# Kernel optimization log

Hardware: AMD Instinct MI355X
Metric: run time of the kernel (lower is better)

The kernel has to match this reference:

```python
import jax, jax.numpy as jnp
import numpy as np

N, M, E = 100000, 500, 300000
XS, GS, OUT, HEADS = 100, 100, 100, 2
SLOPE = 0.2
EPS = 1e-12


def l2norm(x, axis):
    n = jnp.linalg.norm(x, axis=axis, keepdims=True)
    return x / jnp.maximum(n, EPS)


def gat_layer(h_ijk, ends, n, W, att):
    # W: [heads*out, in_dim] (no bias); att: [1, heads, out]
    heads, out = att.shape[1], att.shape[2]
    c = (h_ijk @ W.T).reshape(-1, heads, out)               # [E, H, D]
    a = jnp.sum(att * c, axis=2, keepdims=True)             # [E, H, 1]
    e = jnp.exp(-jax.nn.leaky_relu(a, SLOPE))
    denom = jax.ops.segment_sum(e, ends, num_segments=n)    # [n, H, 1]
    alpha = e / denom[ends]                                 # segment softmax (dropout=eval/identity)
    h = jax.ops.segment_sum(alpha * c, ends, num_segments=n)  # [n, H, D]
    h = jax.nn.elu(h)
    h = l2norm(h, axis=2)
    return h.reshape(n, heads * out)


def merge_layer(h_in, h_out, Wi, bi, Wo, bo, Wl, bl):
    hi = h_in @ Wi.T + bi
    ho = h_out @ Wo.T + bo
    lam = jax.nn.sigmoid(jnp.concatenate([hi, ho], axis=1) @ Wl.T + bl)
    h = lam * hi + (1.0 - lam) * ho
    return l2norm(jax.nn.elu(h), axis=1)


def setup_inputs() -> dict:
    key = jax.random.key(0)
    ks = jax.random.split(key, 24)
    D = HEADS * OUT  # 200
    in1 = 2 * XS + GS   # 300
    in2 = 3 * D         # 600
    s = 0.05
    return {
        'edge_idx': jax.random.randint(ks[0], (2, E), 0, N),
        'edge_type': jax.random.randint(ks[1], (E,), 0, M),
        'path_idx': jax.random.randint(ks[2], (2, 8), 0, N),
        'path_type': jax.random.randint(ks[3], (2, 8), 0, M),
        'use_path': 0,
        'x': jax.random.normal(ks[4], (N, XS), jnp.float32),
        'g': jax.random.normal(ks[5], (M, GS), jnp.float32),
        'W_in1': s * jax.random.normal(ks[6], (D, in1), jnp.float32),
        'att_in1': s * jax.random.normal(ks[7], (1, HEADS, OUT), jnp.float32),
        'W_out1': s * jax.random.normal(ks[8], (D, in1), jnp.float32),
        'att_out1': s * jax.random.normal(ks[9], (1, HEADS, OUT), jnp.float32),
        'Wi1': s * jax.random.normal(ks[10], (D, D), jnp.float32), 'bi1': jnp.zeros((D,), jnp.float32),
        'Wo1': s * jax.random.normal(ks[11], (D, D), jnp.float32), 'bo1': jnp.zeros((D,), jnp.float32),
        'Wl1': s * jax.random.normal(ks[12], (1, 2 * D), jnp.float32), 'bl1': jnp.zeros((1,), jnp.float32),
        'Wr': s * jax.random.normal(ks[13], (D, GS), jnp.float32), 'br': jnp.zeros((D,), jnp.float32),
        'Wf': s * jax.random.normal(ks[14], (D, in1), jnp.float32), 'bf': jnp.zeros((D,), jnp.float32),
        'W_in2': s * jax.random.normal(ks[15], (D, in2), jnp.float32),
        'att_in2': s * jax.random.normal(ks[16], (1, 1, D), jnp.float32),
        'W_out2': s * jax.random.normal(ks[17], (D, in2), jnp.float32),
        'att_out2': s * jax.random.normal(ks[18], (1, 1, D), jnp.float32),
        'Wi2': s * jax.random.normal(ks[19], (D, D), jnp.float32), 'bi2': jnp.zeros((D,), jnp.float32),
        'Wo2': s * jax.random.normal(ks[20], (D, D), jnp.float32), 'bo2': jnp.zeros((D,), jnp.float32),
        'Wl2': s * jax.random.normal(ks[21], (1, 2 * D), jnp.float32), 'bl2': jnp.zeros((1,), jnp.float32),
        'W_ent': s * jax.random.normal(ks[22], (D, XS), jnp.float32),
    }


def reference(edge_idx, edge_type, path_idx, path_type, use_path, x, g,
              W_in1, att_in1, W_out1, att_out1, Wi1, bi1, Wo1, bo1, Wl1, bl1,
              Wr, br, Wf, bf,
              W_in2, att_in2, W_out2, att_out2, Wi2, bi2, Wo2, bo2, Wl2, bl2,
              W_ent):
    n, m = x.shape[0], g.shape[0]
    x = l2norm(x, axis=1)  # x_initial is renormalized each forward
    row, col = edge_idx[0], edge_idx[1]
    # hop 1: gather-concat per-edge features [E, 2*XS+GS]
    h_ijk = jnp.concatenate([x[row], x[col], g[edge_type]], axis=1)
    h_in = gat_layer(h_ijk, col, n, W_in1, att_in1)
    h_out = gat_layer(h_ijk, row, n, W_out1, att_out1)
    h = merge_layer(h_in, h_out, Wi1, bi1, Wo1, bo1, Wl1, bl1)
    # relation layer
    g_edges = jax.ops.segment_sum(h_ijk, edge_type, num_segments=m)
    g_edges = jax.nn.elu(l2norm(g_edges, axis=1))
    g_prime = (g @ Wr.T + br) + (g_edges @ Wf.T + bf)
    # hop 2
    h_ijk2 = jnp.concatenate([h[row], h[col], g_prime[edge_type]], axis=1)
    h_in2 = gat_layer(h_ijk2, col, n, W_in2, att_in2)
    h_out2 = gat_layer(h_ijk2, row, n, W_out2, att_out2)
    h = merge_layer(h_in2, h_out2, Wi2, bi2, Wo2, bo2, Wl2, bl2)
    # entity residual layer
    h_prime = x @ W_ent.T + h
    return h_prime
```

## Files before the change

kernel.cpp:

```cpp
#include <hip/hip_runtime.h>
#include <cstddef>
#include <cstdint>

#define WSLOPE 0.2f
#define WEPS 1e-12f

typedef __attribute__((ext_vector_type(8))) short bf16x8;
typedef __attribute__((ext_vector_type(4))) float f32x4;
typedef __attribute__((ext_vector_type(2))) float f32x2;

__device__ __forceinline__ float waveSum(float v) {
#pragma unroll
    for (int off = 32; off > 0; off >>= 1) v += __shfl_xor(v, off, 64);
    return v;
}
__device__ __forceinline__ float rowSum16(float v) {
#pragma unroll
    for (int off = 8; off > 0; off >>= 1) v += __shfl_xor(v, off, 64);
    return v;
}
__device__ __forceinline__ float eluf(float v) { return v > 0.f ? v : expm1f(v); }
__device__ __forceinline__ short f2bf(float f) {
    union { float f; uint32_t u; } v; v.f = f;
    uint32_t r = v.u + 0x7FFF + ((v.u >> 16) & 1);
    return (short)(r >> 16);
}
__device__ __forceinline__ float bf2f(short s) {
    union { uint32_t u; float f; } v; v.u = ((uint32_t)(uint16_t)s) << 16;
    return v.f;
}

__global__ void k_nodeprep(const float* __restrict__ x, short* __restrict__ xnb,
                           const float* __restrict__ wai, const float* __restrict__ wao,
                           f32x4* __restrict__ ndi, f32x4* __restrict__ ndo, int N) {
    int wid = blockIdx.x * 4 + (threadIdx.x >> 6);
    int lane = threadIdx.x & 63;
    if (wid >= N) return;
    const float* p = x + (size_t)wid * 100;
    float a0 = p[lane];
    float a1 = (lane < 36) ? p[lane + 64] : 0.f;
    float ss = waveSum(a0 * a0 + a1 * a1);
    float inv = 1.f / fmaxf(sqrtf(ss), WEPS);
    float f0 = a0 * inv, f1 = a1 * inv;
    short* xb = xnb + (size_t)wid * 112;
    xb[lane] = f2bf(f0);
    if (lane < 36) xb[64 + lane] = f2bf(f1);
    else if (lane < 48) xb[64 + lane] = 0;
    float rI[2], cI[2], rO[2], cO[2];
#pragma unroll
    for (int h = 0; h < 2; ++h) {
        const float* wi = wai + h * 300;
        const float* wo = wao + h * 300;
        float ri = f0 * wi[lane] + f1 * wi[lane + 64];
        float ci = f0 * wi[100 + lane] + f1 * wi[100 + lane + 64];
        float ro = f0 * wo[lane] + f1 * wo[lane + 64];
        float co = f0 * wo[100 + lane] + f1 * wo[100 + lane + 64];
        rI[h] = waveSum(ri); cI[h] = waveSum(ci); rO[h] = waveSum(ro); cO[h] = waveSum(co);
    }
    if (lane == 0) {
        ndi[wid] = f32x4{rI[0], rI[1], cI[0], cI[1]};
        ndo[wid] = f32x4{rO[0], rO[1], cO[0], cO[1]};
    }
}

__global__ void k_gprep(const float* __restrict__ g, short* __restrict__ gbf,
                        short* __restrict__ gcomb,
                        const float* __restrict__ wai, const float* __restrict__ wao,
                        float* __restrict__ gdi, float* __restrict__ gdo, int M) {
    int m = blockIdx.x * 4 + (threadIdx.x >> 6);
    int lane = threadIdx.x & 63;
    if (m >= M) return;
    const float* gm = g + (size_t)m * 100;
    float v0 = gm[lane];
    float v1 = (lane < 36) ? gm[lane + 64] : 0.f;
    short b0 = f2bf(v0), b1 = (lane < 36) ? f2bf(v1) : (short)0;
    short* gb = gbf + (size_t)m * 112;
    gb[lane] = b0;
    if (lane < 48) gb[64 + lane] = (lane < 36) ? b1 : (short)0;
    short* gc = gcomb + (size_t)m * 416;
    gc[lane] = b0;
    if (lane < 48) gc[64 + lane] = (lane < 36) ? b1 : (short)0;
    float s0 = v0 * wai[200 + lane];
    float s1 = v0 * wai[500 + lane];
    float s2 = v0 * wao[200 + lane];
    float s3 = v0 * wao[500 + lane];
    if (lane < 36) {
        s0 += v1 * wai[264 + lane]; s1 += v1 * wai[564 + lane];
        s2 += v1 * wao[264 + lane]; s3 += v1 * wao[564 + lane];
    }
    s0 = waveSum(s0); s1 = waveSum(s1); s2 = waveSum(s2); s3 = waveSum(s3);
    if (lane == 0) { gdi[m * 2] = s0; gdi[m * 2 + 1] = s1; gdo[m * 2] = s2; gdo[m * 2 + 1] = s3; }
}

__global__ void k_count(const int* __restrict__ keys, int* __restrict__ cnt, int n) {
    int i = blockIdx.x * 256 + threadIdx.x;
    if (i < n) atomicAdd(&cnt[keys[i]], 1);
}

#define SCAN_CHUNK 2048
__global__ void k_blocksum(const int* __restrict__ cnt, int* __restrict__ bsum, int n) {
    __shared__ int sh[256];
    int b = blockIdx.x, t = threadIdx.x;
    int base = b * SCAN_CHUNK;
    int s = 0;
    for (int i = t; i < SCAN_CHUNK; i += 256) { int idx = base + i; if (idx < n) s += cnt[idx]; }
    sh[t] = s; __syncthreads();
    for (int off = 128; off > 0; off >>= 1) { if (t < off) sh[t] += sh[t + off]; __syncthreads(); }
    if (t == 0) bsum[b] = sh[0];
}

__global__ void k_scanwrite(const int* __restrict__ cnt, const int* __restrict__ bsum,
                            int* __restrict__ offs, int* __restrict__ cur, int n, int nb) {
    __shared__ int sh[256];
    __shared__ int sbase;
    int b = blockIdx.x, t = threadIdx.x;
    if (t == 0) { int s = 0; for (int i = 0; i < b; ++i) s += bsum[i]; sbase = s; }
    __syncthreads();
    int base = b * SCAN_CHUNK;
    int loc[8]; int ts = 0;
#pragma unroll
    for (int i = 0; i < 8; ++i) { int idx = base + t * 8 + i; int v = (idx < n) ? cnt[idx] : 0; loc[i] = ts; ts += v; }
    sh[t] = ts; __syncthreads();
    for (int off = 1; off < 256; off <<= 1) {
        int v = (t >= off) ? sh[t - off] : 0;
        __syncthreads();
        sh[t] += v;
        __syncthreads();
    }
    int excl = (t == 0) ? 0 : sh[t - 1];
    int gbase = sbase + excl;
#pragma unroll
    for (int i = 0; i < 8; ++i) {
        int idx = base + t * 8 + i;
        if (idx < n) { offs[idx] = gbase + loc[i]; cur[idx] = gbase + loc[i]; }
    }
    if (b == nb - 1 && t == 255) offs[n] = sbase + sh[255];
}

__global__ void k_scatter3(const int* __restrict__ keys, const int* __restrict__ other,
                           const int* __restrict__ et, int* __restrict__ cur,
                           int* __restrict__ nbrS, int* __restrict__ etS,
                           int* __restrict__ keyS, int n) {
    int i = blockIdx.x * 256 + threadIdx.x;
    if (i < n) {
        int p = atomicAdd(&cur[keys[i]], 1);
        nbrS[p] = other[i];
        etS[p] = et[i];
        keyS[p] = keys[i];
    }
}

__global__ void k_scatter2(const int* __restrict__ keys, int* __restrict__ cur,
                           int* __restrict__ rs, int* __restrict__ cs,
                           const int* __restrict__ row, const int* __restrict__ col, int n) {
    int i = blockIdx.x * 256 + threadIdx.x;
    if (i < n) {
        int p = atomicAdd(&cur[keys[i]], 1);
        rs[p] = row[i];
        cs[p] = col[i];
    }
}

__global__ void k_watt(const float* __restrict__ att, const float* __restrict__ W,
                       float* __restrict__ wa, int H, int DH, int K) {
    int id = blockIdx.x * 256 + threadIdx.x;
    if (id >= H * K) return;
    int h = id / K, k = id % K;
    float s = 0.f;
    for (int j = 0; j < DH; ++j) s += att[h * DH + j] * W[(size_t)(h * DH + j) * K + k];
    wa[id] = s;
}

__global__ void k_ewh1(const int* __restrict__ nbi, const int* __restrict__ kyi,
                       const int* __restrict__ eti,
                       const int* __restrict__ nbo, const int* __restrict__ kyo,
                       const int* __restrict__ eto,
                       const f32x4* __restrict__ ndi, const f32x4* __restrict__ ndo,
                       const float* __restrict__ gdi, const float* __restrict__ gdo,
                       float* __restrict__ ewi, float* __restrict__ ewo, int E) {
    int id = blockIdx.x * 256 + threadIdx.x;
    int tot = E * 2;
    if (id >= 2 * tot) return;
    if (id < tot) {
        int p = id >> 1, h = id & 1;
        f32x4 n1 = ndi[nbi[p]];
        f32x4 n2 = ndi[kyi[p]];
        float a = (h ? n1.y : n1.x) + (h ? n2.w : n2.z) + gdi[eti[p] * 2 + h];
        float lr = a > 0.f ? a : WSLOPE * a;
        ewi[id] = expf(-lr);
    } else {
        int id2 = id - tot;
        int p = id2 >> 1, h = id2 & 1;
        f32x4 n1 = ndo[nbo[p]];
        f32x4 n2 = ndo[kyo[p]];
        float a = (h ? n1.w : n1.z) + (h ? n2.y : n2.x) + gdo[eto[p] * 2 + h];
        float lr = a > 0.f ? a : WSLOPE * a;
        ewo[id2] = expf(-lr);
    }
}

__global__ void k_ewh2(const int* __restrict__ nbi, const int* __restrict__ kyi,
                       const int* __restrict__ eti,
                       const int* __restrict__ nbo, const int* __restrict__ kyo,
                       const int* __restrict__ eto,
                       const f32x4* __restrict__ nd2, const f32x2* __restrict__ gd2,
                       float* __restrict__ ewi, float* __restrict__ ewo, int E) {
    int id = blockIdx.x * 256 + threadIdx.x;
    if (id >= 2 * E) return;
    if (id < E) {
        f32x4 n1 = nd2[nbi[id]];
        f32x4 n2 = nd2[kyi[id]];
        float a = n1.x + n2.y + gd2[eti[id]].x;
        float lr = a > 0.f ? a : WSLOPE * a;
        ewi[id] = expf(-lr);
    } else {
        int p = id - E;
        f32x4 n1 = nd2[nbo[p]];
        f32x4 n2 = nd2[kyo[p]];
        float a = n1.w + n2.z + gd2[eto[p]].y;
        float lr = a > 0.f ? a : WSLOPE * a;
        ewo[p] = expf(-lr);
    }
}

template<bool HOP2>
__global__ void k_agg(const int* __restrict__ offs, const int* __restrict__ nbrS,
                      const int* __restrict__ etS, const float* __restrict__ ewS,
                      const short* __restrict__ featB, const short* __restrict__ gB,
                      short* __restrict__ A, int n0, int n1) {
    constexpr int H = HOP2 ? 1 : 2;
    constexpr int LDA = 448;
    constexpr int FW = HOP2 ? 224 : 112;
    constexpr int GW = HOP2 ? 224 : 112;
    int node = n0 + blockIdx.x * 4 + (threadIdx.x >> 6);
    int lane = threadIdx.x & 63;
    if (node >= n1) return;
    int o = offs[node];
    int deg = offs[node + 1] - o;
    float va[7];
#pragma unroll
    for (int m = 0; m < 7; ++m) va[m] = 0.f;
    if (deg > 0) {
        float s0 = 0.f, s1 = 0.f;
        for (int i = lane; i < deg; i += 64) {
            s0 += ewS[(size_t)(o + i) * H];
            if (H == 2) s1 += ewS[(size_t)(o + i) * H + 1];
        }
        s0 = waveSum(s0);
        float rd0 = 1.f / s0, rd1 = rd0;
        if (H == 2) { s1 = waveSum(s1); rd1 = 1.f / s1; }
        for (int j = 0; j < deg; ++j) {
            float a0 = ewS[(size_t)(o + j) * H] * rd0;
            float a1 = (H == 2) ? ewS[(size_t)(o + j) * H + 1] * rd1 : a0;
            int nbr = nbrS[o + j];
            int et = etS[o + j];
            const short* fr = featB + (size_t)nbr * FW;
            const short* gr = gB + (size_t)et * GW;
            if (!HOP2) {
#pragma unroll
                for (int m = 0; m < 7; ++m) {
                    int d = lane + m * 64;
                    if (d < 100) va[m] += a0 * bf2f(fr[d]);
                    else if (d < 200) va[m] += a1 * bf2f(fr[d - 100]);
                    else if (d < 300) va[m] += a0 * bf2f(gr[d - 200]);
                    else if (d < 400) va[m] += a1 * bf2f(gr[d - 300]);
                }
            } else {
#pragma unroll
                for (int m = 0; m < 7; ++m) {
                    int d = lane + m * 64;
                    if (d < 200) va[m] += a0 * bf2f(fr[d]);
                    else if (d < 424) va[m] += a0 * bf2f(gr[d - 200]);
                }
            }
        }
    }
    size_t rb = (size_t)(node - n0);
    short* Ar = A + rb * LDA;
    if (!HOP2) {
#pragma unroll
        for (int m = 0; m < 7; ++m) {
            int d = lane + m * 64;
            if (d < 400) {
                int col = d < 100 ? d : (d < 200 ? d + 12 : (d < 300 ? d + 24 : d + 36));
                Ar[col] = f2bf(va[m]);
            }
        }
        if (lane < 48) { int q = lane / 12; int rm = lane - q * 12; Ar[q * 112 + 100 + rm] = 0; }
    } else {
#pragma unroll
        for (int m = 0; m < 7; ++m) {
            int d = lane + m * 64;
            if (d < 424) Ar[d < 200 ? d : d + 24] = f2bf(va[m]);
        }
        if (lane < 24) Ar[200 + lane] = 0;
    }
}

template<int KS_S, int H>
__launch_bounds__(256)
__global__ void k_mgemm_post(const short* __restrict__ A, const short* __restrict__ Wb,
                             const short* __restrict__ selfB, int selfLD,
                             const int* __restrict__ offs,
                             short* __restrict__ post, int rows) {
    constexpr int KS_A = 14;
    constexpr int LDW = (KS_A + KS_S) * 32;
    const int t = threadIdx.x;
    const int wv = t >> 6, l = t & 63;
    const int lhi = l >> 4, llo = l & 15;
    const int rbase = blockIdx.x * 64 + wv * 16;
    const int ra = rbase + llo;
    const int deg = (ra < rows) ? (offs[ra + 1] - offs[ra]) : 0;
    f32x4 acc[13];
#pragma unroll
    for (int j = 0; j < 13; ++j) acc[j] = f32x4{0.f, 0.f, 0.f, 0.f};
    const short* arow = A + (size_t)ra * 448 + lhi * 8;
#pragma unroll
    for (int kt = 0; kt < KS_A; ++kt) {
        bf16x8 a = *(const bf16x8*)(arow + kt * 32);
#pragma unroll
        for (int j = 0; j < 13; ++j) {
            bf16x8 b = *(const bf16x8*)(Wb + (size_t)(j * 16 + llo) * LDW + kt * 32 + lhi * 8);
            acc[j] = __builtin_amdgcn_mfma_f32_16x16x32_bf16(a, b, acc[j], 0, 0, 0);
        }
    }
    const short* srow = selfB + (size_t)ra * selfLD + lhi * 8;
#pragma unroll
    for (int kt = 0; kt < KS_S; ++kt) {
        bf16x8 a;
        if (deg > 0) a = *(const bf16x8*)(srow + kt * 32);
        else a = bf16x8{0, 0, 0, 0, 0, 0, 0, 0};
#pragma unroll
        for (int j = 0; j < 13; ++j) {
            bf16x8 b = *(const bf16x8*)(Wb + (size_t)(j * 16 + llo) * LDW + (KS_A + kt) * 32 + lhi * 8);
            acc[j] = __builtin_amdgcn_mfma_f32_16x16x32_bf16(a, b, acc[j], 0, 0, 0);
        }
    }
    const int r0 = rbase + lhi * 4;
#pragma unroll
    for (int e = 0; e < 4; ++e) {
        int r = r0 + e;
        if (r >= rows) continue;
        float v[13];
        float s0 = 0.f, s1 = 0.f;
#pragma unroll
        for (int j = 0; j < 13; ++j) {
            int d = j * 16 + llo;
            if (d < 200) {
                float xv = eluf(acc[j][e]);
                v[j] = xv;
                if (H == 1 || d < 100) s0 += xv * xv; else s1 += xv * xv;
            }
        }
        s0 = rowSum16(s0);
        float inv0 = 1.f / fmaxf(sqrtf(s0), WEPS);
        float inv1 = inv0;
        if (H == 2) { s1 = rowSum16(s1); inv1 = 1.f / fmaxf(sqrtf(s1), WEPS); }
        short* pr = post + (size_t)r * 224;
#pragma unroll
        for (int j = 0; j < 13; ++j) {
            int d = j * 16 + llo;
            if (d < 200) pr[d] = f2bf(v[j] * ((H == 2 && d >= 100) ? inv1 : inv0));
        }
    }
}

template<bool HOP1>
__launch_bounds__(512)
__global__ void k_mergemm2(const short* __restrict__ pA, const short* __restrict__ pB,
                           const short* __restrict__ Wi, const short* __restrict__ Wo,
                           const float* __restrict__ bi, const float* __restrict__ bo,
                           const float* __restrict__ Wl, const float* __restrict__ bl,
                           const short* __restrict__ xnb, const short* __restrict__ Went,
                           float* __restrict__ outf, short* __restrict__ h1b,
                           const float* __restrict__ wa2i, const float* __restrict__ wa2o,
                           f32x4* __restrict__ nd2,
                           int rows) {
    __shared__ float lpS[2][64];
    __shared__ float ssS[2][64];
    __shared__ float dotS[2][64][4];
    const int t = threadIdx.x;
    const int wvAll = t >> 6;
    const int rg = wvAll >> 1;
    const int half = wvAll & 1;
    const int l = t & 63;
    const int lhi = l >> 4, llo = l & 15;
    const int jbase = half * 7;
    const int rbase = blockIdx.x * 64 + rg * 16;
    f32x4 accA[7], accB[7];
#pragma unroll
    for (int j = 0; j < 7; ++j) { accA[j] = f32x4{0.f, 0.f, 0.f, 0.f}; accB[j] = f32x4{0.f, 0.f, 0.f, 0.f}; }
    const short* pa = pA + (size_t)(rbase + llo) * 224 + lhi * 8;
    const short* pb = pB + (size_t)(rbase + llo) * 224 + lhi * 8;
#pragma unroll
    for (int kt = 0; kt < 7; ++kt) {
        bf16x8 a1 = *(const bf16x8*)(pa + kt * 32);
        bf16x8 a2 = *(const bf16x8*)(pb + kt * 32);
#pragma unroll
        for (int j = 0; j < 7; ++j) {
            if (jbase + j < 13) {
                bf16x8 b1 = *(const bf16x8*)(Wi + (size_t)((jbase + j) * 16 + llo) * 224 + kt * 32 + lhi * 8);
                accA[j] = __builtin_amdgcn_mfma_f32_16x16x32_bf16(a1, b1, accA[j], 0, 0, 0);
                bf16x8 b2 = *(const bf16x8*)(Wo + (size_t)((jbase + j) * 16 + llo) * 224 + kt * 32 + lhi * 8);
                accB[j] = __builtin_amdgcn_mfma_f32_16x16x32_bf16(a2, b2, accB[j], 0, 0, 0);
            }
        }
    }
    f32x4 accR[7];
    if (!HOP1) {
#pragma unroll
        for (int j = 0; j < 7; ++j) accR[j] = f32x4{0.f, 0.f, 0.f, 0.f};
        const short* xr = xnb + (size_t)(rbase + llo) * 112 + lhi * 8;
#pragma unroll
        for (int kt = 0; kt < 4; ++kt) {
            bf16x8 a = *(const bf16x8*)(xr + kt * 32);
#pragma unroll
            for (int j = 0; j < 7; ++j) {
                if (jbase + j < 13) {
                    bf16x8 b = *(const bf16x8*)(Went + (size_t)((jbase + j) * 16 + llo) * 128 + kt * 32 + lhi * 8);
                    accR[j] = __builtin_amdgcn_mfma_f32_16x16x32_bf16(a, b, accR[j], 0, 0, 0);
                }
            }
        }
    }
    const int r0 = rbase + lhi * 4;
    const int rrb = rg * 16 + lhi * 4;
    float blv = bl[0];
#pragma unroll
    for (int e = 0; e < 4; ++e) {
        float lp = 0.f;
#pragma unroll
        for (int j = 0; j < 7; ++j) {
            int d = (jbase + j) * 16 + llo;
            if (jbase + j < 13 && d < 200)
                lp += Wl[d] * (accA[j][e] + bi[d]) + Wl[200 + d] * (accB[j][e] + bo[d]);
        }
        lp = rowSum16(lp);
        if (llo == 0) lpS[half][rrb + e] = lp;
    }
    __syncthreads();
    float lamAll[4];
#pragma unroll
    for (int e = 0; e < 4; ++e) {
        float lam = 1.f / (1.f + expf(-(lpS[0][rrb + e] + lpS[1][rrb + e] + blv)));
        lamAll[e] = lam;
        float ss = 0.f;
#pragma unroll
        for (int j = 0; j < 7; ++j) {
            int d = (jbase + j) * 16 + llo;
            if (jbase + j < 13 && d < 200) {
                float vi = accA[j][e] + bi[d];
                float vo = accB[j][e] + bo[d];
                float hv = eluf(lam * vi + (1.f - lam) * vo);
                ss += hv * hv;
            }
        }
        ss = rowSum16(ss);
        if (llo == 0) ssS[half][rrb + e] = ss;
    }
    __syncthreads();
#pragma unroll
    for (int e = 0; e < 4; ++e) {
        int r = r0 + e;
        if (r >= rows) continue;
        float inv = 1.f / fmaxf(sqrtf(ssS[0][rrb + e] + ssS[1][rrb + e]), WEPS);
        float lam = lamAll[e];
        float ri = 0.f, ci = 0.f, ro = 0.f, co = 0.f;
#pragma unroll
        for (int j = 0; j < 7; ++j) {
            if (jbase + j >= 13) continue;
            int d = (jbase + j) * 16 + llo;
            if (d < 200) {
                float vi = accA[j][e] + bi[d];
                float vo = accB[j][e] + bo[d];
                float val = eluf(lam * vi + (1.f - lam) * vo) * inv;
                if (HOP1) {
                    h1b[(size_t)r * 224 + d] = f2bf(val);
                    ri += val * wa2i[d]; ci += val * wa2i[200 + d];
                    ro += val * wa2o[d]; co += val * wa2o[200 + d];
                } else {
                    outf[(size_t)r * 200 + d] = val + accR[j][e];
                }
            } else if (HOP1) {
                h1b[(size_t)r * 224 + d] = 0;
            }
        }
        if (HOP1) {
            if (half) h1b[(size_t)r * 224 + 208 + llo] = 0;
            ri = rowSum16(ri); ci = rowSum16(ci); ro = rowSum16(ro); co = rowSum16(co);
            if (llo == 0) {
                dotS[half][rrb + e][0] = ri; dotS[half][rrb + e][1] = ci;
                dotS[half][rrb + e][2] = ro; dotS[half][rrb + e][3] = co;
            }
        }
    }
    if (HOP1) {
        __syncthreads();
        if (half == 0 && llo == 0) {
#pragma unroll
            for (int e = 0; e < 4; ++e) {
                int r = r0 + e;
                if (r < rows) {
                    nd2[r] = f32x4{dotS[0][rrb + e][0] + dotS[1][rrb + e][0],
                                   dotS[0][rrb + e][1] + dotS[1][rrb + e][1],
                                   dotS[0][rrb + e][2] + dotS[1][rrb + e][2],
                                   dotS[0][rrb + e][3] + dotS[1][rrb + e][3]};
                }
            }
        }
    }
}

__launch_bounds__(256)
__global__ void k_mgemm_rel(const short* __restrict__ A, const short* __restrict__ Wb,
                            const float* __restrict__ brf,
                            short* __restrict__ gout, const float* __restrict__ wai,
                            const float* __restrict__ wao,
                            f32x2* __restrict__ gd2, int rows) {
    constexpr int KSTEPS = 13, LDW = KSTEPS * 32;
    const int t = threadIdx.x;
    const int wv = t >> 6, l = t & 63;
    const int lhi = l >> 4, llo = l & 15;
    const int rbase = blockIdx.x * 64 + wv * 16;
    f32x4 acc[13];
#pragma unroll
    for (int j = 0; j < 13; ++j) acc[j] = f32x4{0.f, 0.f, 0.f, 0.f};
    const short* arow = A + (size_t)(rbase + llo) * 416 + lhi * 8;
#pragma unroll
    for (int kt = 0; kt < KSTEPS; ++kt) {
        bf16x8 a = *(const bf16x8*)(arow + kt * 32);
#pragma unroll
        for (int j = 0; j < 13; ++j) {
            bf16x8 b = *(const bf16x8*)(Wb + (size_t)(j * 16 + llo) * LDW + kt * 32 + lhi * 8);
            acc[j] = __builtin_amdgcn_mfma_f32_16x16x32_bf16(a, b, acc[j], 0, 0, 0);
        }
    }
    const int r0 = rbase + lhi * 4;
#pragma unroll
    for (int e = 0; e < 4; ++e) {
        int r = r0 + e;
        if (r >= rows) continue;
        short* pr = gout + (size_t)r * 224;
        float gi = 0.f, go = 0.f;
#pragma unroll
        for (int j = 0; j < 13; ++j) {
            int d = j * 16 + llo;
            if (d < 200) {
                float val = acc[j][e] + brf[d];
                pr[d] = f2bf(val);
                gi += val * wai[400 + d];
                go += val * wao[400 + d];
            } else {
                pr[d] = 0;
            }
        }
        pr[208 + llo] = 0;
        gi = rowSum16(gi); go = rowSum16(go);
        if (llo == 0) gd2[r] = f32x2{gi, go};
    }
}

__global__ void k_prepw(const float* __restrict__ W, int ldW, int koff, int Klen, int span,
                        int mode, short* __restrict__ Wb, int ldWb, int dst) {
    int id = blockIdx.x * 256 + threadIdx.x;
    int tot = 208 * span;
    if (id >= tot) return;
    int d = id / span, k = id - d * span;
    float v = 0.f;
    if (d < 200) {
        if (mode == 0) { if (k < Klen) v = W[(size_t)d * ldW + koff + k]; }
        else { int h = d / 100; int kk = k - h * 112; if (kk >= 0 && kk < Klen) v = W[(size_t)d * ldW + koff + kk]; }
    }
    Wb[(size_t)d * ldWb + dst + k] = f2bf(v);
}

__global__ void k_prepwrf(const float* __restrict__ Wr, const float* __restrict__ Wf,
                          short* __restrict__ Wb) {
    int id = blockIdx.x * 256 + threadIdx.x;
    if (id >= 208 * 416) return;
    int d = id / 416, k = id - d * 416;
    float v = 0.f;
    if (d < 200) {
        if (k < 100) v = Wr[(size_t)d * 100 + k];
        else if (k >= 112 && k < 412) v = Wf[(size_t)d * 300 + (k - 112)];
    }
    Wb[id] = f2bf(v);
}

__global__ void k_brf(const float* __restrict__ br, const float* __restrict__ bf,
                      float* __restrict__ brf) {
    int d = threadIdx.x;
    if (d < 200) brf[d] = br[d] + bf[d];
}

__global__ void k_gedges_b(const int* __restrict__ rsT, const int* __restrict__ csT,
                           const int* __restrict__ offsT,
                           const short* __restrict__ xnb,
                           const short* __restrict__ gbf, short* __restrict__ gcomb, int M) {
    __shared__ float red[6];
    int m = blockIdx.x, t = threadIdx.x;
    int o = offsT[m];
    int deg = offsT[m + 1] - o;
    float acc = 0.f;
    if (t < 128) {
        int d = t; bool ok = d < 100;
        for (int i = 0; i < deg; ++i) {
            int r = rsT[o + i];
            if (ok) acc += bf2f(xnb[(size_t)r * 112 + d]);
        }
    } else if (t < 256) {
        int d = t - 128; bool ok = d < 100;
        for (int i = 0; i < deg; ++i) {
            int c = csT[o + i];
            if (ok) acc += bf2f(xnb[(size_t)c * 112 + d]);
        }
    } else {
        int d = t - 256;
        if (d < 100) acc = (float)deg * bf2f(gbf[(size_t)m * 112 + d]);
    }
    float sq = waveSum(acc * acc);
    if ((t & 63) == 0) red[t >> 6] = sq;
    __syncthreads();
    float s2 = red[0] + red[1] + red[2] + red[3] + red[4] + red[5];
    float inv = 1.f / fmaxf(sqrtf(s2), WEPS);
    short* orow = gcomb + (size_t)m * 416 + 112;
    if (t < 128) {
        if (t < 100) orow[t] = f2bf(eluf(acc * inv));
    } else if (t < 256) {
        int d = t - 128;
        if (d < 100) orow[100 + d] = f2bf(eluf(acc * inv));
    } else {
        int d = t - 256;
        if (d < 100) orow[200 + d] = f2bf(eluf(acc * inv));
        else if (d < 104) orow[200 + d] = 0;
    }
}

extern "C" void kernel_launch(void* const* d_in, const int* in_sizes, int n_in,
                              void* d_out, int out_size, void* d_ws, size_t ws_size,
                              hipStream_t stream) {
    const int* eidx   = (const int*)d_in[0];
    const int* etype  = (const int*)d_in[1];
    const float* x    = (const float*)d_in[5];
    const float* g    = (const float*)d_in[6];
    const float* W_in1  = (const float*)d_in[7];
    const float* att_in1 = (const float*)d_in[8];
    const float* W_out1 = (const float*)d_in[9];
    const float* att_out1 = (const float*)d_in[10];
    const float* Wi1 = (const float*)d_in[11]; const float* bi1 = (const float*)d_in[12];
    const float* Wo1 = (const float*)d_in[13]; const float* bo1 = (const float*)d_in[14];
    const float* Wl1 = (const float*)d_in[15]; const float* bl1 = (const float*)d_in[16];
    const float* Wr  = (const float*)d_in[17]; const float* br  = (const float*)d_in[18];
    const float* Wf  = (const float*)d_in[19]; const float* bf  = (const float*)d_in[20];
    const float* W_in2  = (const float*)d_in[21]; const float* att_in2 = (const float*)d_in[22];
    const float* W_out2 = (const float*)d_in[23]; const float* att_out2 = (const float*)d_in[24];
    const float* Wi2 = (const float*)d_in[25]; const float* bi2 = (const float*)d_in[26];
    const float* Wo2 = (const float*)d_in[27]; const float* bo2 = (const float*)d_in[28];
    const float* Wl2 = (const float*)d_in[29]; const float* bl2 = (const float*)d_in[30];
    const float* W_ent = (const float*)d_in[31];

    const int E = in_sizes[1];
    const int N = in_sizes[5] / 100;
    const int M = in_sizes[6] / 100;
    const int Mr = (M + 63) & ~63;
    float* out = (float*)d_out;
    const int* row = eidx;
    const int* col = eidx + E;

    char* w = (char*)d_ws;
    size_t off_b = 0;
    auto alloc = [&](size_t bytes) -> void* {
        void* p = w + off_b;
        off_b += (bytes + 255) & ~(size_t)255;
        return p;
    };
    short* h1_bf = (short*)alloc((size_t)(N + 64) * 224 * 2);
    short* xn_bf = (short*)alloc((size_t)(N + 64) * 112 * 2);
    short* g_bf  = (short*)alloc((size_t)M * 112 * 2);
    short* gp_bf = (short*)alloc((size_t)Mr * 224 * 2);
    int* offs_in = (int*)alloc((size_t)(N + 1) * 4);
    int* offs_out= (int*)alloc((size_t)(N + 1) * 4);
    int* offsT   = (int*)alloc((size_t)(M + 1) * 4);
    int* nbrS_in = (int*)alloc((size_t)E * 4);
    int* etS_in  = (int*)alloc((size_t)E * 4);
    int* keyS_in = (int*)alloc((size_t)E * 4);
    int* nbrS_out= (int*)alloc((size_t)E * 4);
    int* etS_out = (int*)alloc((size_t)E * 4);
    int* keyS_out= (int*)alloc((size_t)E * 4);
    int* rsT     = (int*)alloc((size_t)E * 4);
    int* csT     = (int*)alloc((size_t)E * 4);
    int* cnt     = (int*)alloc((size_t)N * 4);
    int* cur     = (int*)alloc((size_t)N * 4);
    int* bsum    = (int*)alloc((size_t)64 * 4);
    float* wa1_in = (float*)alloc((size_t)640 * 4);
    float* wa1_out= (float*)alloc((size_t)640 * 4);
    float* wa2_in = (float*)alloc((size_t)640 * 4);
    float* wa2_out= (float*)alloc((size_t)640 * 4);
    f32x4* nd1i  = (f32x4*)alloc((size_t)N * 16);
    f32x4* nd1o  = (f32x4*)alloc((size_t)N * 16);
    f32x4* nd2   = (f32x4*)alloc((size_t)N * 16);
    float* gdot_in = (float*)alloc((size_t)M * 2 * 4);
    float* gdot_out= (float*)alloc((size_t)M * 2 * 4);
    f32x2* gd2   = (f32x2*)alloc((size_t)M * 8);
    float* ewS_in  = (float*)alloc((size_t)E * 2 * 4);
    float* ewS_out = (float*)alloc((size_t)E * 2 * 4);
    short* gcomb   = (short*)alloc((size_t)Mr * 416 * 2);
    short* Wc_in1  = (short*)alloc((size_t)208 * 576 * 2);
    short* Wc_out1 = (short*)alloc((size_t)208 * 576 * 2);
    short* Wc_in2  = (short*)alloc((size_t)208 * 672 * 2);
    short* Wc_out2 = (short*)alloc((size_t)208 * 672 * 2);
    short* Wm_i1   = (short*)alloc((size_t)208 * 224 * 2);
    short* Wm_o1   = (short*)alloc((size_t)208 * 224 * 2);
    short* Wm_i2   = (short*)alloc((size_t)208 * 224 * 2);
    short* Wm_o2   = (short*)alloc((size_t)208 * 224 * 2);
    short* Wb_ent  = (short*)alloc((size_t)208 * 128 * 2);
    short* Wrf_b   = (short*)alloc((size_t)208 * 416 * 2);
    float* brf     = (float*)alloc((size_t)200 * 4);

    if (off_b >= ws_size) return;
    size_t rem = ws_size - off_b;
    long long Cll = (long long)(rem / 1920);
    long long Nr64 = ((long long)N + 63) & ~63LL;
    int C = (int)(Cll > Nr64 ? Nr64 : Cll);
    C &= ~63;
    if (C < 64) return;
    short* Ac    = (short*)alloc((size_t)C * 448 * 2);
    short* postA = (short*)alloc((size_t)C * 224 * 2);
    short* postB = (short*)alloc((size_t)C * 224 * 2);
    if (off_b > ws_size) return;

    const int gE = (E + 255) / 256;
    const int gN4 = (N + 3) / 4;
    const int gM4 = (M + 3) / 4;
    const int gM64 = (M + 63) / 64;

    hipMemsetAsync(postA, 0, (size_t)C * 224 * 2, stream);
    hipMemsetAsync(postB, 0, (size_t)C * 224 * 2, stream);
    hipMemsetAsync(xn_bf + (size_t)N * 112, 0, (size_t)64 * 112 * 2, stream);
    hipMemsetAsync(h1_bf + (size_t)N * 224, 0, (size_t)64 * 224 * 2, stream);

    auto gsp = [](int span) { return (208 * span + 255) / 256; };
    k_prepw<<<gsp(224), 256, 0, stream>>>(W_in1, 300, 0, 100, 224, 1, Wc_in1, 576, 0);
    k_prepw<<<gsp(224), 256, 0, stream>>>(W_in1, 300, 200, 100, 224, 1, Wc_in1, 576, 224);
    k_prepw<<<gsp(128), 256, 0, stream>>>(W_in1, 300, 100, 100, 128, 0, Wc_in1, 576, 448);
    k_prepw<<<gsp(224), 256, 0, stream>>>(W_out1, 300, 100, 100, 224, 1, Wc_out1, 576, 0);
    k_prepw<<<gsp(224), 256, 0, stream>>>(W_out1, 300, 200, 100, 224, 1, Wc_out1, 576, 224);
    k_prepw<<<gsp(128), 256, 0, stream>>>(W_out1, 300, 0, 100, 128, 0, Wc_out1, 576, 448);
    k_prepw<<<gsp(224), 256, 0, stream>>>(W_in2, 600, 0, 200, 224, 0, Wc_in2, 672, 0);
    k_prepw<<<gsp(224), 256, 0, stream>>>(W_in2, 600, 400, 200, 224, 0, Wc_in2, 672, 224);
    k_prepw<<<gsp(224), 256, 0, stream>>>(W_in2, 600, 200, 200, 224, 0, Wc_in2, 672, 448);
    k_prepw<<<gsp(224), 256, 0, stream>>>(W_out2, 600, 200, 200, 224, 0, Wc_out2, 672, 0);
    k_prepw<<<gsp(224), 256, 0, stream>>>(W_out2, 600, 400, 200, 224, 0, Wc_out2, 672, 224);
    k_prepw<<<gsp(224), 256, 0, stream>>>(W_out2, 600, 0, 200, 224, 0, Wc_out2, 672, 448);
    k_prepw<<<gsp(224), 256, 0, stream>>>(Wi1, 200, 0, 200, 224, 0, Wm_i1, 224, 0);
    k_prepw<<<gsp(224), 256, 0, stream>>>(Wo1, 200, 0, 200, 224, 0, Wm_o1, 224, 0);
    k_prepw<<<gsp(224), 256, 0, stream>>>(Wi2, 200, 0, 200, 224, 0, Wm_i2, 224, 0);
    k_prepw<<<gsp(224), 256, 0, stream>>>(Wo2, 200, 0, 200, 224, 0, Wm_o2, 224, 0);
    k_prepw<<<gsp(128), 256, 0, stream>>>(W_ent, 100, 0, 100, 128, 0, Wb_ent, 128, 0);
    k_prepwrf<<<gsp(416), 256, 0, stream>>>(Wr, Wf, Wrf_b);
    k_brf<<<1, 256, 0, stream>>>(br, bf, brf);

    int nbN = (N + SCAN_CHUNK - 1) / SCAN_CHUNK;
    int nbM = (M + SCAN_CHUNK - 1) / SCAN_CHUNK;
    hipMemsetAsync(cnt, 0, (size_t)N * 4, stream);
    k_count<<<gE, 256, 0, stream>>>(col, cnt, E);
    k_blocksum<<<nbN, 256, 0, stream>>>(cnt, bsum, N);
    k_scanwrite<<<nbN, 256, 0, stream>>>(cnt, bsum, offs_in, cur, N, nbN);
    k_scatter3<<<gE, 256, 0, stream>>>(col, row, etype, cur, nbrS_in, etS_in, keyS_in, E);

    hipMemsetAsync(cnt, 0, (size_t)N * 4, stream);
    k_count<<<gE, 256, 0, stream>>>(row, cnt, E);
    k_blocksum<<<nbN, 256, 0, stream>>>(cnt, bsum, N);
    k_scanwrite<<<nbN, 256, 0, stream>>>(cnt, bsum, offs_out, cur, N, nbN);
    k_scatter3<<<gE, 256, 0, stream>>>(row, col, etype, cur, nbrS_out, etS_out, keyS_out, E);

    hipMemsetAsync(cnt, 0, (size_t)M * 4, stream);
    k_count<<<gE, 256, 0, stream>>>(etype, cnt, E);
    k_blocksum<<<nbM, 256, 0, stream>>>(cnt, bsum, M);
    k_scanwrite<<<nbM, 256, 0, stream>>>(cnt, bsum, offsT, cur, M, nbM);
    k_scatter2<<<gE, 256, 0, stream>>>(etype, cur, rsT, csT, row, col, E);

    k_watt<<<(600 + 255) / 256, 256, 0, stream>>>(att_in1, W_in1, wa1_in, 2, 100, 300);
    k_watt<<<(600 + 255) / 256, 256, 0, stream>>>(att_out1, W_out1, wa1_out, 2, 100, 300);
    k_watt<<<(600 + 255) / 256, 256, 0, stream>>>(att_in2, W_in2, wa2_in, 1, 200, 600);
    k_watt<<<(600 + 255) / 256, 256, 0, stream>>>(att_out2, W_out2, wa2_out, 1, 200, 600);

    k_nodeprep<<<gN4, 256, 0, stream>>>(x, xn_bf, wa1_in, wa1_out, nd1i, nd1o, N);
    k_gprep<<<gM4, 256, 0, stream>>>(g, g_bf, gcomb, wa1_in, wa1_out, gdot_in, gdot_out, M);
    k_ewh1<<<(2 * E * 2 + 255) / 256, 256, 0, stream>>>(nbrS_in, keyS_in, etS_in,
                                                        nbrS_out, keyS_out, etS_out,
                                                        nd1i, nd1o, gdot_in, gdot_out,
                                                        ewS_in, ewS_out, E);

    for (int n0 = 0; n0 < N; n0 += C) {
        int rows = (N - n0 < C) ? (N - n0) : C;
        int n1 = n0 + rows;
        int ga = (rows + 3) / 4;
        int gb = (rows + 63) / 64;
        k_agg<false><<<ga, 256, 0, stream>>>(offs_in, nbrS_in, etS_in, ewS_in, xn_bf, g_bf, Ac, n0, n1);
        k_mgemm_post<4, 2><<<gb, 256, 0, stream>>>(Ac, Wc_in1, xn_bf + (size_t)n0 * 112, 112,
                                                   offs_in + n0, postA, rows);
        k_agg<false><<<ga, 256, 0, stream>>>(offs_out, nbrS_out, etS_out, ewS_out, xn_bf, g_bf, Ac, n0, n1);
        k_mgemm_post<4, 2><<<gb, 256, 0, stream>>>(Ac, Wc_out1, xn_bf + (size_t)n0 * 112, 112,
                                                   offs_out + n0, postB, rows);
        k_mergemm2<true><<<gb, 512, 0, stream>>>(postA, postB, Wm_i1, Wm_o1, bi1, bo1, Wl1, bl1,
                                                 nullptr, nullptr,
                                                 nullptr, h1_bf + (size_t)n0 * 224,
                                                 wa2_in, wa2_out, nd2 + n0, rows);
    }

    k_gedges_b<<<M, 384, 0, stream>>>(rsT, csT, offsT, xn_bf, g_bf, gcomb, M);
    k_mgemm_rel<<<gM64, 256, 0, stream>>>(gcomb, Wrf_b, brf, gp_bf, wa2_in, wa2_out, gd2, M);

    k_ewh2<<<(2 * E + 255) / 256, 256, 0, stream>>>(nbrS_in, keyS_in, etS_in,
                                                    nbrS_out, keyS_out, etS_out,
                                                    nd2, gd2, ewS_in, ewS_out, E);

    for (int n0 = 0; n0 < N; n0 += C) {
        int rows = (N - n0 < C) ? (N - n0) : C;
        int n1 = n0 + rows;
        int ga = (rows + 3) / 4;
        int gb = (rows + 63) / 64;
        k_agg<true><<<ga, 256, 0, stream>>>(offs_in, nbrS_in, etS_in, ewS_in, h1_bf, gp_bf, Ac, n0, n1);
        k_mgemm_post<7, 1><<<gb, 256, 0, stream>>>(Ac, Wc_in2, h1_bf + (size_t)n0 * 224, 224,
                                                   offs_in + n0, postA, rows);
        k_agg<true><<<ga, 256, 0, stream>>>(offs_out, nbrS_out, etS_out, ewS_out, h1_bf, gp_bf, Ac, n0, n1);
        k_mgemm_post<7, 1><<<gb, 256, 0, stream>>>(Ac, Wc_out2, h1_bf + (size_t)n0 * 224, 224,
                                                   offs_out + n0, postB, rows);
        k_mergemm2<false><<<gb, 512, 0, stream>>>(postA, postB, Wm_i2, Wm_o2, bi2, bo2, Wl2, bl2,
                                                  xn_bf + (size_t)n0 * 112, Wb_ent,
                                                  out + (size_t)n0 * 200, nullptr,
                                                  nullptr, nullptr, nullptr, rows);
    }
}
```

Measured before the change: 2.504 ms.

## Fuse out-direction post GEMM into merge kernel via shared-memory staging

Replaces the separate out-direction post-GEMM kernel plus merge kernel with a single kernel. It computes the out-GAT projection, ELU and per-head L2 norm in registers and stages the normalized bf16 rows in LDS for the merge GEMM. This removes one launch per chunk and the postB global write and read, and frees workspace so chunks can be larger. The cost is more LDS and registers per 512-thread block and an extra block-wide barrier, which may reduce occupancy.

```diff
diff --git a/kernel.cpp b/kernel.cpp
--- a/kernel.cpp
+++ b/kernel.cpp
@@ -365,17 +365,23 @@
     }
 }
 
-template<bool HOP1>
+template<int KS_S, int H, bool HOP1>
 __launch_bounds__(512)
-__global__ void k_mergemm2(const short* __restrict__ pA, const short* __restrict__ pB,
-                           const short* __restrict__ Wi, const short* __restrict__ Wo,
-                           const float* __restrict__ bi, const float* __restrict__ bo,
-                           const float* __restrict__ Wl, const float* __restrict__ bl,
-                           const short* __restrict__ xnb, const short* __restrict__ Went,
-                           float* __restrict__ outf, short* __restrict__ h1b,
-                           const float* __restrict__ wa2i, const float* __restrict__ wa2o,
-                           f32x4* __restrict__ nd2,
-                           int rows) {
+__global__ void k_postmerge(const short* __restrict__ Ac, const short* __restrict__ Wc,
+                            const short* __restrict__ selfB, int selfLD,
+                            const int* __restrict__ offs,
+                            const short* __restrict__ pA,
+                            const short* __restrict__ Wi, const short* __restrict__ Wo,
+                            const float* __restrict__ bi, const float* __restrict__ bo,
+                            const float* __restrict__ Wl, const float* __restrict__ bl,
+                            const short* __restrict__ xnb, const short* __restrict__ Went,
+                            float* __restrict__ outf, short* __restrict__ h1b,
+                            const float* __restrict__ wa2i, const float* __restrict__ wa2o,
+                            f32x4* __restrict__ nd2, int rows) {
+    constexpr int KS_A = 14;
+    constexpr int LDW = (KS_A + KS_S) * 32;
+    __shared__ short pBl[64][232];
+    __shared__ float redS[2][64][2];
     __shared__ float lpS[2][64];
     __shared__ float ssS[2][64];
     __shared__ float dotS[2][64][4];
@@ -387,15 +393,88 @@
     const int lhi = l >> 4, llo = l & 15;
     const int jbase = half * 7;
     const int rbase = blockIdx.x * 64 + rg * 16;
+    const int rrbase = rg * 16;
+
+    float v1[4][7];
+    {
+        const int ra = rbase + llo;
+        const int deg = (ra < rows) ? (offs[ra + 1] - offs[ra]) : 0;
+        f32x4 acc[7];
+#pragma unroll
+        for (int j = 0; j < 7; ++j) acc[j] = f32x4{0.f, 0.f, 0.f, 0.f};
+        const short* arow = Ac + (size_t)ra * 448 + lhi * 8;
+#pragma unroll
+        for (int kt = 0; kt < KS_A; ++kt) {
+            bf16x8 a = *(const bf16x8*)(arow + kt * 32);
+#pragma unroll
+            for (int j = 0; j < 7; ++j) {
+                if (jbase + j < 13) {
+                    bf16x8 b = *(const bf16x8*)(Wc + (size_t)((jbase + j) * 16 + llo) * LDW + kt * 32 + lhi * 8);
+                    acc[j] = __builtin_amdgcn_mfma_f32_16x16x32_bf16(a, b, acc[j], 0, 0, 0);
+                }
+            }
+        }
+        const short* srow = selfB + (size_t)ra * selfLD + lhi * 8;
+#pragma unroll
+        for (int kt = 0; kt < KS_S; ++kt) {
+            bf16x8 a;
+            if (deg > 0) a = *(const bf16x8*)(srow + kt * 32);
+            else a = bf16x8{0, 0, 0, 0, 0, 0, 0, 0};
+#pragma unroll
+            for (int j = 0; j < 7; ++j) {
+                if (jbase + j < 13) {
+                    bf16x8 b = *(const bf16x8*)(Wc + (size_t)((jbase + j) * 16 + llo) * LDW + (KS_A + kt) * 32 + lhi * 8);
+                    acc[j] = __builtin_amdgcn_mfma_f32_16x16x32_bf16(a, b, acc[j], 0, 0, 0);
+                }
+            }
+        }
+#pragma unroll
+        for (int e = 0; e < 4; ++e) {
+            float s0 = 0.f, s1 = 0.f;
+#pragma unroll
+            for (int j = 0; j < 7; ++j) {
+                int d = (jbase + j) * 16 + llo;
+                if (jbase + j < 13 && d < 200) {
+                    float xv = eluf(acc[j][e]);
+                    v1[e][j] = xv;
+                    if (H == 1 || d < 100) s0 += xv * xv; else s1 += xv * xv;
+                }
+            }
+            s0 = rowSum16(s0);
+            if (H == 2) s1 = rowSum16(s1);
+            if (llo == 0) { redS[half][rrbase + lhi * 4 + e][0] = s0; redS[half][rrbase + lhi * 4 + e][1] = s1; }
+        }
+    }
+    __syncthreads();
+#pragma unroll
+    for (int e = 0; e < 4; ++e) {
+        int rr = rrbase + lhi * 4 + e;
+        float s0 = redS[0][rr][0] + redS[1][rr][0];
+        float inv0 = 1.f / fmaxf(sqrtf(s0), WEPS);
+        float inv1 = inv0;
+        if (H == 2) {
+            float s1 = redS[0][rr][1] + redS[1][rr][1];
+            inv1 = 1.f / fmaxf(sqrtf(s1), WEPS);
+        }
+#pragma unroll
+        for (int j = 0; j < 7; ++j) {
+            if (jbase + j >= 13) continue;
+            int d = (jbase + j) * 16 + llo;
+            if (d < 200) pBl[rr][d] = f2bf(v1[e][j] * ((H == 2 && d >= 100) ? inv1 : inv0));
+            else pBl[rr][d] = 0;
+        }
+        if (half) pBl[rr][208 + llo] = 0;
+    }
+    __syncthreads();
+
     f32x4 accA[7], accB[7];
 #pragma unroll
     for (int j = 0; j < 7; ++j) { accA[j] = f32x4{0.f, 0.f, 0.f, 0.f}; accB[j] = f32x4{0.f, 0.f, 0.f, 0.f}; }
     const short* pa = pA + (size_t)(rbase + llo) * 224 + lhi * 8;
-    const short* pb = pB + (size_t)(rbase + llo) * 224 + lhi * 8;
 #pragma unroll
     for (int kt = 0; kt < 7; ++kt) {
         bf16x8 a1 = *(const bf16x8*)(pa + kt * 32);
-        bf16x8 a2 = *(const bf16x8*)(pb + kt * 32);
+        bf16x8 a2 = *(const bf16x8*)(&pBl[rrbase + llo][kt * 32 + lhi * 8]);
 #pragma unroll
         for (int j = 0; j < 7; ++j) {
             if (jbase + j < 13) {
@@ -424,7 +503,7 @@
         }
     }
     const int r0 = rbase + lhi * 4;
-    const int rrb = rg * 16 + lhi * 4;
+    const int rrb = rrbase + lhi * 4;
     float blv = bl[0];
 #pragma unroll
     for (int e = 0; e < 4; ++e) {
@@ -719,14 +798,13 @@
 
     if (off_b >= ws_size) return;
     size_t rem = ws_size - off_b;
-    long long Cll = (long long)(rem / 1920);
+    long long Cll = (long long)(rem / 1472);
     long long Nr64 = ((long long)N + 63) & ~63LL;
     int C = (int)(Cll > Nr64 ? Nr64 : Cll);
     C &= ~63;
     if (C < 64) return;
     short* Ac    = (short*)alloc((size_t)C * 448 * 2);
     short* postA = (short*)alloc((size_t)C * 224 * 2);
-    short* postB = (short*)alloc((size_t)C * 224 * 2);
     if (off_b > ws_size) return;
 
     const int gE = (E + 255) / 256;
@@ -735,7 +813,6 @@
     const int gM64 = (M + 63) / 64;
 
     hipMemsetAsync(postA, 0, (size_t)C * 224 * 2, stream);
-    hipMemsetAsync(postB, 0, (size_t)C * 224 * 2, stream);
     hipMemsetAsync(xn_bf + (size_t)N * 112, 0, (size_t)64 * 112 * 2, stream);
     hipMemsetAsync(h1_bf + (size_t)N * 224, 0, (size_t)64 * 224 * 2, stream);
 
@@ -801,12 +878,12 @@
         k_mgemm_post<4, 2><<<gb, 256, 0, stream>>>(Ac, Wc_in1, xn_bf + (size_t)n0 * 112, 112,
                                                    offs_in + n0, postA, rows);
         k_agg<false><<<ga, 256, 0, stream>>>(offs_out, nbrS_out, etS_out, ewS_out, xn_bf, g_bf, Ac, n0, n1);
-        k_mgemm_post<4, 2><<<gb, 256, 0, stream>>>(Ac, Wc_out1, xn_bf + (size_t)n0 * 112, 112,
-                                                   offs_out + n0, postB, rows);
-        k_mergemm2<true><<<gb, 512, 0, stream>>>(postA, postB, Wm_i1, Wm_o1, bi1, bo1, Wl1, bl1,
-                                                 nullptr, nullptr,
-                                                 nullptr, h1_bf + (size_t)n0 * 224,
-                                                 wa2_in, wa2_out, nd2 + n0, rows);
+        k_postmerge<4, 2, true><<<gb, 512, 0, stream>>>(Ac, Wc_out1, xn_bf + (size_t)n0 * 112, 112,
+                                                        offs_out + n0, postA,
+                                                        Wm_i1, Wm_o1, bi1, bo1, Wl1, bl1,
+                                                        nullptr, nullptr,
+                                                        nullptr, h1_bf + (size_t)n0 * 224,
+                                                        wa2_in, wa2_out, nd2 + n0, rows);
     }
 
     k_gedges_b<<<M, 384, 0, stream>>>(rsT, csT, offsT, xn_bf, g_bf, gcomb, M);
@@ -825,11 +902,11 @@
         k_mgemm_post<7, 1><<<gb, 256, 0, stream>>>(Ac, Wc_in2, h1_bf + (size_t)n0 * 224, 224,
                                                    offs_in + n0, postA, rows);
         k_agg<true><<<ga, 256, 0, stream>>>(offs_out, nbrS_out, etS_out, ewS_out, h1_bf, gp_bf, Ac, n0, n1);
-        k_mgemm_post<7, 1><<<gb, 256, 0, stream>>>(Ac, Wc_out2, h1_bf + (size_t)n0 * 224, 224,
-                                                   offs_out + n0, postB, rows);
-        k_mergemm2<false><<<gb, 512, 0, stream>>>(postA, postB, Wm_i2, Wm_o2, bi2, bo2, Wl2, bl2,
-                                                  xn_bf + (size_t)n0 * 112, Wb_ent,
-                                                  out + (size_t)n0 * 200, nullptr,
-                                                  nullptr, nullptr, nullptr, rows);
-    }
-}
+        k_postmerge<7, 1, false><<<gb, 512, 0, stream>>>(Ac, Wc_out2, h1_bf + (size_t)n0 * 224, 224,
+                                                         offs_out + n0, postA,
+                                                         Wm_i2, Wm_o2, bi2, bo2, Wl2, bl2,
+                                                         xn_bf + (size_t)n0 * 112, Wb_ent,
+                                                         out + (size_t)n0 * 200, nullptr,
+                                                         nullptr, nullptr, nullptr, rows);
+    }
+}
```

Result: no change. 2.502 ms (-0.1%).
